# Performance work log

Hardware: AMD Instinct MI355X
Metric: run time of the kernel (lower is better)

The kernel has to match this reference:

```python
import jax, jax.numpy as jnp
import numpy as np

D = 1024
H = 16
DH = D // H  # 64
SCALE = DH ** (-0.5)

def setup_inputs() -> dict:
    key = jax.random.key(0)
    k1, k2, k3, k4, k5 = jax.random.split(key, 5)
    x = jax.random.normal(k1, (4, 2048, D), dtype=jnp.float32)
    w_qkv = jax.random.normal(k2, (D, 3 * D), dtype=jnp.float32) * (D ** -0.5)
    b_qkv = jax.random.normal(k3, (3 * D,), dtype=jnp.float32) * 0.02
    w_out = jax.random.normal(k4, (D, D), dtype=jnp.float32) * (D ** -0.5)
    b_out = jax.random.normal(k5, (D,), dtype=jnp.float32) * 0.02
    return {"x": x, "w_qkv": w_qkv, "b_qkv": b_qkv, "w_out": w_out, "b_out": b_out}

def reference(x, w_qkv, b_qkv, w_out, b_out):
    B, S, C = x.shape
    qkv = x @ w_qkv + b_qkv                          # [B,S,3D]
    qkv = qkv.reshape(B, S, 3, H, DH)
    qkv = jnp.transpose(qkv, (0, 3, 2, 1, 4))        # [B,H,3,S,DH]
    q, k, v = qkv[:, :, 0], qkv[:, :, 1], qkv[:, :, 2]
    q = q * SCALE
    scores = jnp.einsum('bhqd,bhkd->bhqk', q, k)     # [B,H,S,S]
    attn = jax.nn.softmax(scores.astype(jnp.float32), axis=-1).astype(scores.dtype)
    out = jnp.einsum('bhqk,bhkd->bhqd', attn, v)     # [B,H,S,DH]
    out = jnp.transpose(out, (0, 2, 1, 3)).reshape(B, S, C)
    return out @ w_out + b_out
```

## Files before the change

kernel.cpp:

```cpp
#include <hip/hip_runtime.h>

#define D_ 1024
#define H_ 16
#define DH_ 64
#define S_ 2048
#define B_ 4
#define N_ (B_*S_)
#define M3_ 3072
#define QSC_ 0.18033688011112042f

typedef _Float16 f16;
typedef _Float16 f16x8 __attribute__((ext_vector_type(8)));
typedef _Float16 f16x4 __attribute__((ext_vector_type(4)));
typedef _Float16 f16x2 __attribute__((ext_vector_type(2)));
typedef __fp16   h16x2 __attribute__((ext_vector_type(2)));
typedef float    f32x4 __attribute__((ext_vector_type(4)));

typedef __attribute__((address_space(1))) void gvoid;
typedef __attribute__((address_space(3))) void lvoid;

__device__ __forceinline__ void gl16(const f16* g, f16* l) {
    __builtin_amdgcn_global_load_lds((gvoid*)g, (lvoid*)l, 16, 0, 0);
}

__device__ __forceinline__ f16x2 pk_cvt(float a, float b) {
#if __has_builtin(__builtin_amdgcn_cvt_pkrtz)
    h16x2 t = __builtin_amdgcn_cvt_pkrtz(a, b);
    return __builtin_bit_cast(f16x2, t);
#else
    f16x2 r; r[0] = (f16)a; r[1] = (f16)b; return r;
#endif
}

__global__ __launch_bounds__(256) void cvt_x_kernel(const float* __restrict__ in,
                                                    f16* __restrict__ out) {
    size_t i = ((size_t)blockIdx.x * 256 + threadIdx.x) * 4;
    float4 f = *reinterpret_cast<const float4*>(in + i);
    f16x4 o;
    o[0] = (f16)f.x; o[1] = (f16)f.y; o[2] = (f16)f.z; o[3] = (f16)f.w;
    *reinterpret_cast<f16x4*>(out + i) = o;
}

__global__ __launch_bounds__(256) void wt_cvt_kernel(const float* __restrict__ in,
                                                     f16* __restrict__ out,
                                                     int K, int Nc) {
    __shared__ float tile[32][33];
    int tx = threadIdx.x & 31, ty = threadIdx.x >> 5;
    int c = blockIdx.x * 32 + tx;
    #pragma unroll
    for (int i = 0; i < 4; i++) {
        int r = blockIdx.y * 32 + ty + i * 8;
        tile[ty + i * 8][tx] = in[(size_t)r * Nc + c];
    }
    __syncthreads();
    #pragma unroll
    for (int i = 0; i < 4; i++) {
        int r2 = blockIdx.x * 32 + ty + i * 8;
        int c2 = blockIdx.y * 32 + tx;
        out[(size_t)r2 * K + c2] = (f16)tile[tx][ty + i * 8];
    }
}

__global__ __launch_bounds__(256) void gemm_qkv_kernel(
        const f16* __restrict__ A, const f16* __restrict__ Bt,
        const float* __restrict__ bias,
        f16* __restrict__ qo, f16* __restrict__ ko, f16* __restrict__ vTo) {
    __shared__ __align__(16) f16 As[128 * 32];
    __shared__ __align__(16) f16 Bs[128 * 32];
    const int tid  = threadIdx.x;
    const int lane = tid & 63, w = tid >> 6;
    const int quad = lane >> 4, lrow = lane & 15;
    const int wm = (w & 1) * 64, wn = (w >> 1) * 64;
    const int n0 = blockIdx.x * 128, m0 = blockIdx.y * 128;

    f32x4 acc[4][4];
    #pragma unroll
    for (int i = 0; i < 4; i++)
        #pragma unroll
        for (int j = 0; j < 4; j++) acc[i][j] = {0.f, 0.f, 0.f, 0.f};

    const int ar0 = tid >> 2, ap0 = tid & 3;
    const f16* Ag0 = A  + (size_t)(n0 + ar0) * D_ + ap0 * 8;
    const f16* Ag1 = Ag0 + (size_t)64 * D_;
    const f16* Bg0 = Bt + (size_t)(m0 + ar0) * D_ + ap0 * 8;
    const f16* Bg1 = Bg0 + (size_t)64 * D_;
    f16* Asl = As + tid * 8;
    f16* Bsl = Bs + tid * 8;

    for (int kt = 0; kt < D_ / 32; kt++) {
        gl16(Ag0 + kt * 32, Asl);
        gl16(Ag1 + kt * 32, Asl + 64 * 32);
        gl16(Bg0 + kt * 32, Bsl);
        gl16(Bg1 + kt * 32, Bsl + 64 * 32);
        __syncthreads();
        f16x8 af[4], bf[4];
        #pragma unroll
        for (int i = 0; i < 4; i++)
            af[i] = *reinterpret_cast<const f16x8*>(&As[(wm + i * 16 + lrow) * 32 + quad * 8]);
        #pragma unroll
        for (int j = 0; j < 4; j++)
            bf[j] = *reinterpret_cast<const f16x8*>(&Bs[(wn + j * 16 + lrow) * 32 + quad * 8]);
        #pragma unroll
        for (int i = 0; i < 4; i++)
            #pragma unroll
            for (int j = 0; j < 4; j++)
                acc[i][j] = __builtin_amdgcn_mfma_f32_16x16x32_f16(af[i], bf[j], acc[i][j], 0, 0, 0);
        __syncthreads();
    }

    #pragma unroll
    for (int j = 0; j < 4; j++) {
        int m   = m0 + wn + j * 16 + lrow;
        int sec = m >> 10;
        int hd  = m & 1023;
        int hh  = hd >> 6, d = hd & 63;
        float bb = bias[m];
        if (sec == 2) {
            #pragma unroll
            for (int i = 0; i < 4; i++) {
                int n = n0 + wm + i * 16 + quad * 4;
                int bidx = n >> 11, s = n & 2047;
                f16x4 o;
                #pragma unroll
                for (int r = 0; r < 4; r++) o[r] = (f16)(acc[i][j][r] + bb);
                *reinterpret_cast<f16x4*>(
                    &vTo[(((size_t)(bidx * H_ + hh)) * DH_ + d) * S_ + s]) = o;
            }
        } else {
            f16* dst = (sec == 0) ? qo : ko;
            float sc = (sec == 0) ? QSC_ : 1.0f;
            #pragma unroll
            for (int i = 0; i < 4; i++) {
                #pragma unroll
                for (int r = 0; r < 4; r++) {
                    int n = n0 + wm + i * 16 + quad * 4 + r;
                    int bidx = n >> 11, s = n & 2047;
                    dst[(((size_t)(bidx * H_ + hh)) * S_ + s) * DH_ + d] =
                        (f16)((acc[i][j][r] + bb) * sc);
                }
            }
        }
    }
}

__global__ __launch_bounds__(256, 4) void attn_kernel(
        const f16* __restrict__ q, const f16* __restrict__ k,
        const f16* __restrict__ vT, f16* __restrict__ ctx) {
    __shared__ __align__(16) f16 Ks[2][64 * 64];
    __shared__ __align__(16) f16 Vs[2][64 * 64];
    const int tid  = threadIdx.x;
    const int lane = tid & 63, w = tid >> 6;
    const int quad = lane >> 4, lrow = lane & 15;
    const int id = blockIdx.x;
    const int bh = id & 63;
    const int q0 = (id >> 6) * 128;
    const int b  = bh >> 4, h = bh & 15;
    const f16* qb = q  + (size_t)bh * S_ * DH_;
    const f16* kb = k  + (size_t)bh * S_ * DH_;
    const f16* vb = vT + (size_t)bh * DH_ * S_;

    f16x8 qf[2][2];
    #pragma unroll
    for (int f = 0; f < 2; f++)
        #pragma unroll
        for (int hf = 0; hf < 2; hf++)
            qf[f][hf] = *reinterpret_cast<const f16x8*>(
                qb + (size_t)(q0 + w * 32 + f * 16 + lrow) * DH_ + hf * 32 + quad * 8);

    f16x8 ones8;
    #pragma unroll
    for (int i = 0; i < 8; i++) ones8[i] = (f16)1.f;

    f32x4 lacc[2];
    f32x4 ot[2][4];
    #pragma unroll
    for (int f = 0; f < 2; f++) {
        lacc[f] = {0.f, 0.f, 0.f, 0.f};
        #pragma unroll
        for (int dj = 0; dj < 4; dj++) ot[f][dj] = {0.f, 0.f, 0.f, 0.f};
    }

    int koff[2], voff[2];
    #pragma unroll
    for (int i = 0; i < 2; i++) {
        int c = i * 256 + tid;
        int s = c >> 3, p = c & 7;
        int g = (s & ~31) | (((s >> 2) & 3) << 3) | (((s >> 4) & 1) << 2) | (s & 3);
        koff[i] = g * DH_ + ((p ^ (s & 7)) * 8);
        voff[i] = s * S_ + ((p ^ (s & 7)) * 8);
    }

    #pragma unroll
    for (int i = 0; i < 2; i++) {
        gl16(kb + koff[i], &Ks[0][(i * 256 + tid) * 8]);
        gl16(vb + voff[i], &Vs[0][(i * 256 + tid) * 8]);
    }
    __syncthreads();

    const int xr0 = (quad ^ (lrow & 7)) * 8;
    const int xr1 = ((quad + 4) ^ (lrow & 7)) * 8;

    union PU { f16x8 v; f16x2 w[4]; };

    const int NT = S_ / 64;
    for (int kt = 0; kt < NT; kt++) {
        const int cur = kt & 1;
        const f16* Kc = Ks[cur];
        const f16* Vc = Vs[cur];

        f32x4 st0[2][2];
        __builtin_amdgcn_s_setprio(1);
        #pragma unroll
        for (int half = 0; half < 2; half++) {
            const int rb = (half * 16 + lrow) * 64;
            const f16x8 k0 = *reinterpret_cast<const f16x8*>(&Kc[rb + xr0]);
            const f16x8 k1 = *reinterpret_cast<const f16x8*>(&Kc[rb + xr1]);
            #pragma unroll
            for (int f = 0; f < 2; f++) {
                f32x4 s = {0.f, 0.f, 0.f, 0.f};
                s = __builtin_amdgcn_mfma_f32_16x16x32_f16(k0, qf[f][0], s, 0, 0, 0);
                s = __builtin_amdgcn_mfma_f32_16x16x32_f16(k1, qf[f][1], s, 0, 0, 0);
                st0[half][f] = s;
            }
        }
        __builtin_amdgcn_s_setprio(0);

        if (kt + 1 < NT) {
            const size_t kv1 = (size_t)(kt + 1) * 64;
            #pragma unroll
            for (int i = 0; i < 2; i++) {
                gl16(kb + kv1 * DH_ + koff[i], &Ks[cur ^ 1][(i * 256 + tid) * 8]);
                gl16(vb + kv1 + voff[i],       &Vs[cur ^ 1][(i * 256 + tid) * 8]);
            }
        }

        PU p0[2];
        #pragma unroll
        for (int half = 0; half < 2; half++)
            #pragma unroll
            for (int f = 0; f < 2; f++) {
                f16x2 lo = pk_cvt(__builtin_amdgcn_exp2f(st0[half][f][0]),
                                  __builtin_amdgcn_exp2f(st0[half][f][1]));
                f16x2 hi = pk_cvt(__builtin_amdgcn_exp2f(st0[half][f][2]),
                                  __builtin_amdgcn_exp2f(st0[half][f][3]));
                p0[f].w[half * 2 + 0] = lo;
                p0[f].w[half * 2 + 1] = hi;
            }

        f32x4 st1[2][2];
        __builtin_amdgcn_s_setprio(1);
        #pragma unroll
        for (int half = 0; half < 2; half++) {
            const int rb = ((2 + half) * 16 + lrow) * 64;
            const f16x8 k0 = *reinterpret_cast<const f16x8*>(&Kc[rb + xr0]);
            const f16x8 k1 = *reinterpret_cast<const f16x8*>(&Kc[rb + xr1]);
            #pragma unroll
            for (int f = 0; f < 2; f++) {
                f32x4 s = {0.f, 0.f, 0.f, 0.f};
                s = __builtin_amdgcn_mfma_f32_16x16x32_f16(k0, qf[f][0], s, 0, 0, 0);
                s = __builtin_amdgcn_mfma_f32_16x16x32_f16(k1, qf[f][1], s, 0, 0, 0);
                st1[half][f] = s;
            }
        }
        __builtin_amdgcn_s_setprio(0);

        f16x8 vf0[4];
        #pragma unroll
        for (int dj = 0; dj < 4; dj++)
            vf0[dj] = *reinterpret_cast<const f16x8*>(
                &Vc[(dj * 16 + lrow) * 64 + ((quad ^ (lrow & 7)) * 8)]);

        __builtin_amdgcn_s_setprio(1);
        #pragma unroll
        for (int dj = 0; dj < 4; dj++)
            #pragma unroll
            for (int f = 0; f < 2; f++)
                ot[f][dj] = __builtin_amdgcn_mfma_f32_16x16x32_f16(vf0[dj], p0[f].v, ot[f][dj], 0, 0, 0);
        #pragma unroll
        for (int f = 0; f < 2; f++)
            lacc[f] = __builtin_amdgcn_mfma_f32_16x16x32_f16(ones8, p0[f].v, lacc[f], 0, 0, 0);
        __builtin_amdgcn_s_setprio(0);

        PU p1[2];
        #pragma unroll
        for (int half = 0; half < 2; half++)
            #pragma unroll
            for (int f = 0; f < 2; f++) {
                f16x2 lo = pk_cvt(__builtin_amdgcn_exp2f(st1[half][f][0]),
                                  __builtin_amdgcn_exp2f(st1[half][f][1]));
                f16x2 hi = pk_cvt(__builtin_amdgcn_exp2f(st1[half][f][2]),
                                  __builtin_amdgcn_exp2f(st1[half][f][3]));
                p1[f].w[half * 2 + 0] = lo;
                p1[f].w[half * 2 + 1] = hi;
            }

        f16x8 vf1[4];
        #pragma unroll
        for (int dj = 0; dj < 4; dj++)
            vf1[dj] = *reinterpret_cast<const f16x8*>(
                &Vc[(dj * 16 + lrow) * 64 + (((4 + quad) ^ (lrow & 7)) * 8)]);

        __builtin_amdgcn_s_setprio(1);
        #pragma unroll
        for (int dj = 0; dj < 4; dj++)
            #pragma unroll
            for (int f = 0; f < 2; f++)
                ot[f][dj] = __builtin_amdgcn_mfma_f32_16x16x32_f16(vf1[dj], p1[f].v, ot[f][dj], 0, 0, 0);
        #pragma unroll
        for (int f = 0; f < 2; f++)
            lacc[f] = __builtin_amdgcn_mfma_f32_16x16x32_f16(ones8, p1[f].v, lacc[f], 0, 0, 0);
        __builtin_amdgcn_s_setprio(0);

        __syncthreads();
    }

    #pragma unroll
    for (int f = 0; f < 2; f++) {
        float inv = 1.0f / lacc[f][0];
        int qrow = q0 + w * 32 + f * 16 + lrow;
        #pragma unroll
        for (int dj = 0; dj < 4; dj++) {
            f16x4 o;
            #pragma unroll
            for (int r = 0; r < 4; r++) o[r] = (f16)(ot[f][dj][r] * inv);
            *reinterpret_cast<f16x4*>(
                &ctx[((size_t)(b * S_ + qrow)) * D_ + h * DH_ + dj * 16 + quad * 4]) = o;
        }
    }
}

__global__ __launch_bounds__(256) void gemm_out_kernel(
        const f16* __restrict__ A, const f16* __restrict__ Bt,
        const float* __restrict__ bias, float* __restrict__ out) {
    __shared__ __align__(16) f16 As[128 * 32];
    __shared__ __align__(16) f16 Bs[128 * 32];
    const int tid  = threadIdx.x;
    const int lane = tid & 63, w = tid >> 6;
    const int quad = lane >> 4, lrow = lane & 15;
    const int wm = (w & 1) * 64, wn = (w >> 1) * 64;
    const int n0 = blockIdx.x * 128, m0 = blockIdx.y * 128;

    f32x4 acc[4][4];
    #pragma unroll
    for (int i = 0; i < 4; i++)
        #pragma unroll
        for (int j = 0; j < 4; j++) acc[i][j] = {0.f, 0.f, 0.f, 0.f};

    const int ar0 = tid >> 2, ap0 = tid & 3;
    const f16* Ag0 = A  + (size_t)(n0 + ar0) * D_ + ap0 * 8;
    const f16* Ag1 = Ag0 + (size_t)64 * D_;
    const f16* Bg0 = Bt + (size_t)(m0 + ar0) * D_ + ap0 * 8;
    const f16* Bg1 = Bg0 + (size_t)64 * D_;
    f16* Asl = As + tid * 8;
    f16* Bsl = Bs + tid * 8;

    for (int kt = 0; kt < D_ / 32; kt++) {
        gl16(Ag0 + kt * 32, Asl);
        gl16(Ag1 + kt * 32, Asl + 64 * 32);
        gl16(Bg0 + kt * 32, Bsl);
        gl16(Bg1 + kt * 32, Bsl + 64 * 32);
        __syncthreads();
        f16x8 af[4], bf[4];
        #pragma unroll
        for (int i = 0; i < 4; i++)
            af[i] = *reinterpret_cast<const f16x8*>(&As[(wm + i * 16 + lrow) * 32 + quad * 8]);
        #pragma unroll
        for (int j = 0; j < 4; j++)
            bf[j] = *reinterpret_cast<const f16x8*>(&Bs[(wn + j * 16 + lrow) * 32 + quad * 8]);
        #pragma unroll
        for (int i = 0; i < 4; i++)
            #pragma unroll
            for (int j = 0; j < 4; j++)
                acc[i][j] = __builtin_amdgcn_mfma_f32_16x16x32_f16(af[i], bf[j], acc[i][j], 0, 0, 0);
        __syncthreads();
    }

    #pragma unroll
    for (int j = 0; j < 4; j++) {
        int m = m0 + wn + j * 16 + lrow;
        float bb = bias[m];
        #pragma unroll
        for (int i = 0; i < 4; i++)
            #pragma unroll
            for (int r = 0; r < 4; r++) {
                int n = n0 + wm + i * 16 + quad * 4 + r;
                out[(size_t)n * D_ + m] = acc[i][j][r] + bb;
            }
    }
}

extern "C" void kernel_launch(void* const* d_in, const int* in_sizes, int n_in,
                              void* d_out, int out_size, void* d_ws, size_t ws_size,
                              hipStream_t stream) {
    (void)in_sizes; (void)n_in; (void)out_size; (void)ws_size;
    const float* x     = (const float*)d_in[0];
    const float* w_qkv = (const float*)d_in[1];
    const float* b_qkv = (const float*)d_in[2];
    const float* w_out = (const float*)d_in[3];
    const float* b_out = (const float*)d_in[4];
    float* out = (float*)d_out;

    char* ws = (char*)d_ws;
    const size_t MB = 1024 * 1024;
    f16* xb    = (f16*)(ws);
    f16* wqkvT = (f16*)(ws + 16 * MB);
    f16* woutT = (f16*)(ws + 22 * MB);
    f16* qs    = (f16*)(ws + 24 * MB);
    f16* kk    = (f16*)(ws + 40 * MB);
    f16* vTb   = (f16*)(ws + 72 * MB);
    f16* ctx   = xb;

    cvt_x_kernel<<<(N_ * D_) / (256 * 4), 256, 0, stream>>>(x, xb);
    wt_cvt_kernel<<<dim3(M3_ / 32, D_ / 32), 256, 0, stream>>>(w_qkv, wqkvT, D_, M3_);
    wt_cvt_kernel<<<dim3(D_ / 32, D_ / 32), 256, 0, stream>>>(w_out, woutT, D_, D_);
    gemm_qkv_kernel<<<dim3(N_ / 128, M3_ / 128), 256, 0, stream>>>(xb, wqkvT, b_qkv, qs, kk, vTb);
    attn_kernel<<<(B_ * H_) * (S_ / 128), 256, 0, stream>>>(qs, kk, vTb, ctx);
    gemm_out_kernel<<<dim3(N_ / 128, D_ / 128), 256, 0, stream>>>(ctx, woutT, b_out, out);
}
```

Baseline: 267.2 us.

## Rework QKV GEMM into 256x256 double-buffered pipeline with swizzled LDS

Reworks the QKV projection GEMM to use 256x256 output tiles with 512 threads. K tiles are double-buffered in LDS, and the global_load_lds prefetch of the next tile overlaps the MFMA work on the current one. LDS chunks are XOR-swizzled to avoid bank conflicts, the 1D block index is remapped for L2 locality, and s_setprio raises priority around the MFMA bursts. This removes the per-iteration full barrier stall and raises arithmetic intensity, in exchange for 128 KB of LDS and a 128-float accumulator per thread, which limits occupancy.

```diff
diff --git a/kernel.cpp b/kernel.cpp
--- a/kernel.cpp
+++ b/kernel.cpp
@@ -61,52 +61,109 @@
     }
 }
 
-__global__ __launch_bounds__(256) void gemm_qkv_kernel(
+__global__ __launch_bounds__(512, 2) void gemm_qkv_kernel(
         const f16* __restrict__ A, const f16* __restrict__ Bt,
         const float* __restrict__ bias,
         f16* __restrict__ qo, f16* __restrict__ ko, f16* __restrict__ vTo) {
-    __shared__ __align__(16) f16 As[128 * 32];
-    __shared__ __align__(16) f16 Bs[128 * 32];
+    __shared__ __align__(16) f16 S[2 * 4 * 8192];
     const int tid  = threadIdx.x;
     const int lane = tid & 63, w = tid >> 6;
     const int quad = lane >> 4, lrow = lane & 15;
-    const int wm = (w & 1) * 64, wn = (w >> 1) * 64;
-    const int n0 = blockIdx.x * 128, m0 = blockIdx.y * 128;
-
-    f32x4 acc[4][4];
-    #pragma unroll
-    for (int i = 0; i < 4; i++)
+    const int G  = w >> 2;
+    const int wn = (w & 3) * 64;
+
+    const int id  = blockIdx.x;
+    const int swz = (id & 7) * 48 + (id >> 3);
+    const int n0 = (swz & 31) * 256;
+    const int m0 = (swz >> 5) * 256;
+
+    f32x4 acc[8][4];
+    #pragma unroll
+    for (int i = 0; i < 8; i++)
         #pragma unroll
         for (int j = 0; j < 4; j++) acc[i][j] = {0.f, 0.f, 0.f, 0.f};
 
-    const int ar0 = tid >> 2, ap0 = tid & 3;
-    const f16* Ag0 = A  + (size_t)(n0 + ar0) * D_ + ap0 * 8;
-    const f16* Ag1 = Ag0 + (size_t)64 * D_;
-    const f16* Bg0 = Bt + (size_t)(m0 + ar0) * D_ + ap0 * 8;
-    const f16* Bg1 = Bg0 + (size_t)64 * D_;
-    f16* Asl = As + tid * 8;
-    f16* Bsl = Bs + tid * 8;
-
-    for (int kt = 0; kt < D_ / 32; kt++) {
-        gl16(Ag0 + kt * 32, Asl);
-        gl16(Ag1 + kt * 32, Asl + 64 * 32);
-        gl16(Bg0 + kt * 32, Bsl);
-        gl16(Bg1 + kt * 32, Bsl + 64 * 32);
-        __syncthreads();
-        f16x8 af[4], bf[4];
-        #pragma unroll
-        for (int i = 0; i < 4; i++)
-            af[i] = *reinterpret_cast<const f16x8*>(&As[(wm + i * 16 + lrow) * 32 + quad * 8]);
-        #pragma unroll
-        for (int j = 0; j < 4; j++)
-            bf[j] = *reinterpret_cast<const f16x8*>(&Bs[(wn + j * 16 + lrow) * 32 + quad * 8]);
-        #pragma unroll
-        for (int i = 0; i < 4; i++)
+    const int c0 = tid, c1 = tid + 512;
+    const int r0 = c0 >> 2, r1 = c1 >> 2;
+    const int g0 = r0 * D_ + (((c0 & 3) ^ (r0 & 3)) * 8);
+    const int g1 = r1 * D_ + (((c1 & 3) ^ (r1 & 3)) * 8);
+    const f16* Ab = A  + (size_t)n0 * D_;
+    const f16* Bb = Bt + (size_t)m0 * D_;
+
+    const int xq8   = (quad ^ (lrow & 3)) * 8;
+    const int abase = (G * 128 + lrow) * 32 + xq8;
+    const int bbase = (wn + lrow) * 32 + xq8;
+
+#define STAGE_QKV(ktn, ck, nb) do {                                          \
+    const int ko_ = (ktn) * 64 + (ck) * 32;                                  \
+    gl16(Ab + ko_ + g0, &S[(((nb) * 4 + (ck)) * 8192) + c0 * 8]);            \
+    gl16(Ab + ko_ + g1, &S[(((nb) * 4 + (ck)) * 8192) + c1 * 8]);            \
+    gl16(Bb + ko_ + g0, &S[(((nb) * 4 + 2 + (ck)) * 8192) + c0 * 8]);        \
+    gl16(Bb + ko_ + g1, &S[(((nb) * 4 + 2 + (ck)) * 8192) + c1 * 8]);        \
+} while (0)
+
+    STAGE_QKV(0, 0, 0);
+    STAGE_QKV(0, 1, 0);
+    asm volatile("s_waitcnt vmcnt(4)" ::: "memory");
+    __builtin_amdgcn_s_barrier();
+    __builtin_amdgcn_sched_barrier(0);
+
+    #pragma unroll 1
+    for (int kt = 0; kt < 15; kt++) {
+        const int buf = kt & 1, nb = buf ^ 1;
+        #pragma unroll
+        for (int ck = 0; ck < 2; ck++) {
+            const f16* Sa = &S[(buf * 4 + ck) * 8192];
+            const f16* Sb = &S[(buf * 4 + 2 + ck) * 8192];
+            f16x8 af[8], bf[4];
+            #pragma unroll
+            for (int i = 0; i < 8; i++)
+                af[i] = *reinterpret_cast<const f16x8*>(Sa + abase + i * 512);
             #pragma unroll
             for (int j = 0; j < 4; j++)
-                acc[i][j] = __builtin_amdgcn_mfma_f32_16x16x32_f16(af[i], bf[j], acc[i][j], 0, 0, 0);
-        __syncthreads();
-    }
+                bf[j] = *reinterpret_cast<const f16x8*>(Sb + bbase + j * 512);
+            STAGE_QKV(kt + 1, ck, nb);
+            __builtin_amdgcn_sched_barrier(0);
+            __builtin_amdgcn_s_setprio(1);
+            #pragma unroll
+            for (int i = 0; i < 8; i++)
+                #pragma unroll
+                for (int j = 0; j < 4; j++)
+                    acc[i][j] = __builtin_amdgcn_mfma_f32_16x16x32_f16(af[i], bf[j], acc[i][j], 0, 0, 0);
+            __builtin_amdgcn_s_setprio(0);
+            asm volatile("s_waitcnt vmcnt(4)" ::: "memory");
+            __builtin_amdgcn_s_barrier();
+            __builtin_amdgcn_sched_barrier(0);
+        }
+    }
+    {
+        const int buf = 1;
+        #pragma unroll
+        for (int ck = 0; ck < 2; ck++) {
+            const f16* Sa = &S[(buf * 4 + ck) * 8192];
+            const f16* Sb = &S[(buf * 4 + 2 + ck) * 8192];
+            f16x8 af[8], bf[4];
+            #pragma unroll
+            for (int i = 0; i < 8; i++)
+                af[i] = *reinterpret_cast<const f16x8*>(Sa + abase + i * 512);
+            #pragma unroll
+            for (int j = 0; j < 4; j++)
+                bf[j] = *reinterpret_cast<const f16x8*>(Sb + bbase + j * 512);
+            __builtin_amdgcn_s_setprio(1);
+            #pragma unroll
+            for (int i = 0; i < 8; i++)
+                #pragma unroll
+                for (int j = 0; j < 4; j++)
+                    acc[i][j] = __builtin_amdgcn_mfma_f32_16x16x32_f16(af[i], bf[j], acc[i][j], 0, 0, 0);
+            __builtin_amdgcn_s_setprio(0);
+            if (ck == 0) {
+                asm volatile("s_waitcnt vmcnt(0)" ::: "memory");
+                __builtin_amdgcn_s_barrier();
+                __builtin_amdgcn_sched_barrier(0);
+            }
+        }
+    }
+#undef STAGE_QKV
 
     #pragma unroll
     for (int j = 0; j < 4; j++) {
@@ -117,8 +174,8 @@
         float bb = bias[m];
         if (sec == 2) {
             #pragma unroll
-            for (int i = 0; i < 4; i++) {
-                int n = n0 + wm + i * 16 + quad * 4;
+            for (int i = 0; i < 8; i++) {
+                int n = n0 + G * 128 + i * 16 + quad * 4;
                 int bidx = n >> 11, s = n & 2047;
                 f16x4 o;
                 #pragma unroll
@@ -130,10 +187,10 @@
             f16* dst = (sec == 0) ? qo : ko;
             float sc = (sec == 0) ? QSC_ : 1.0f;
             #pragma unroll
-            for (int i = 0; i < 4; i++) {
+            for (int i = 0; i < 8; i++) {
                 #pragma unroll
                 for (int r = 0; r < 4; r++) {
-                    int n = n0 + wm + i * 16 + quad * 4 + r;
+                    int n = n0 + G * 128 + i * 16 + quad * 4 + r;
                     int bidx = n >> 11, s = n & 2047;
                     dst[(((size_t)(bidx * H_ + hh)) * S_ + s) * DH_ + d] =
                         (f16)((acc[i][j][r] + bb) * sc);
@@ -413,7 +470,7 @@
     cvt_x_kernel<<<(N_ * D_) / (256 * 4), 256, 0, stream>>>(x, xb);
     wt_cvt_kernel<<<dim3(M3_ / 32, D_ / 32), 256, 0, stream>>>(w_qkv, wqkvT, D_, M3_);
     wt_cvt_kernel<<<dim3(D_ / 32, D_ / 32), 256, 0, stream>>>(w_out, woutT, D_, D_);
-    gemm_qkv_kernel<<<dim3(N_ / 128, M3_ / 128), 256, 0, stream>>>(xb, wqkvT, b_qkv, qs, kk, vTb);
+    gemm_qkv_kernel<<<dim3((N_ / 256) * (M3_ / 256)), 512, 0, stream>>>(xb, wqkvT, b_qkv, qs, kk, vTb);
     attn_kernel<<<(B_ * H_) * (S_ / 128), 256, 0, stream>>>(qs, kk, vTb, ctx);
     gemm_out_kernel<<<dim3(N_ / 128, D_ / 128), 256, 0, stream>>>(ctx, woutT, b_out, out);
 }
```

Result: no change. 272.2 us (+1.9%).

## Double-buffer GEMM LDS tiles, remap blocks per XCD, and merge prep kernels

Applied to the files above, without the earlier changes.

Both GEMM kernels now use double-buffered LDS tiles. The next K-slice is issued via global_load_lds before the current slice's MFMAs, so there is one barrier per iteration instead of two. Blocks are remapped on a 1D grid so that each XCD handles a contiguous group of row tiles, which should improve L2 reuse. The three conversion kernels are merged into a single prep launch, and MFMA sections get s_setprio plus a launch_bounds occupancy hint. The trade-off is doubled LDS per block and a possible race, since the async prefetch writes the other buffer while there is no explicit wait before the barrier.

```diff
diff --git a/kernel.cpp b/kernel.cpp
--- a/kernel.cpp
+++ b/kernel.cpp
@@ -32,46 +32,58 @@
 #endif
 }
 
-__global__ __launch_bounds__(256) void cvt_x_kernel(const float* __restrict__ in,
-                                                    f16* __restrict__ out) {
-    size_t i = ((size_t)blockIdx.x * 256 + threadIdx.x) * 4;
-    float4 f = *reinterpret_cast<const float4*>(in + i);
-    f16x4 o;
-    o[0] = (f16)f.x; o[1] = (f16)f.y; o[2] = (f16)f.z; o[3] = (f16)f.w;
-    *reinterpret_cast<f16x4*>(out + i) = o;
-}
-
-__global__ __launch_bounds__(256) void wt_cvt_kernel(const float* __restrict__ in,
-                                                     f16* __restrict__ out,
-                                                     int K, int Nc) {
+__global__ __launch_bounds__(256) void prep_kernel(
+        const float* __restrict__ x,  f16* __restrict__ xb,
+        const float* __restrict__ wq, f16* __restrict__ wqT,
+        const float* __restrict__ wo, f16* __restrict__ woT) {
     __shared__ float tile[32][33];
+    const int bid = blockIdx.x;
+    if (bid < 8192) {
+        size_t i = ((size_t)bid * 256 + threadIdx.x) * 4;
+        float4 f = *reinterpret_cast<const float4*>(x + i);
+        f16x4 o;
+        o[0] = (f16)f.x; o[1] = (f16)f.y; o[2] = (f16)f.z; o[3] = (f16)f.w;
+        *reinterpret_cast<f16x4*>(xb + i) = o;
+        return;
+    }
+    const float* in; f16* out; int Nc, bx, by;
+    if (bid < 11264) {
+        int t = bid - 8192;  in = wq; out = wqT; Nc = M3_;
+        bx = t % 96; by = t / 96;
+    } else {
+        int t = bid - 11264; in = wo; out = woT; Nc = D_;
+        bx = t & 31; by = t >> 5;
+    }
     int tx = threadIdx.x & 31, ty = threadIdx.x >> 5;
-    int c = blockIdx.x * 32 + tx;
+    int c = bx * 32 + tx;
     #pragma unroll
     for (int i = 0; i < 4; i++) {
-        int r = blockIdx.y * 32 + ty + i * 8;
+        int r = by * 32 + ty + i * 8;
         tile[ty + i * 8][tx] = in[(size_t)r * Nc + c];
     }
     __syncthreads();
     #pragma unroll
     for (int i = 0; i < 4; i++) {
-        int r2 = blockIdx.x * 32 + ty + i * 8;
-        int c2 = blockIdx.y * 32 + tx;
-        out[(size_t)r2 * K + c2] = (f16)tile[tx][ty + i * 8];
-    }
-}
-
-__global__ __launch_bounds__(256) void gemm_qkv_kernel(
+        int r2 = bx * 32 + ty + i * 8;
+        int c2 = by * 32 + tx;
+        out[(size_t)r2 * D_ + c2] = (f16)tile[tx][ty + i * 8];
+    }
+}
+
+__global__ __launch_bounds__(256, 3) void gemm_qkv_kernel(
         const f16* __restrict__ A, const f16* __restrict__ Bt,
         const float* __restrict__ bias,
         f16* __restrict__ qo, f16* __restrict__ ko, f16* __restrict__ vTo) {
-    __shared__ __align__(16) f16 As[128 * 32];
-    __shared__ __align__(16) f16 Bs[128 * 32];
+    __shared__ __align__(16) f16 As[2][128 * 32];
+    __shared__ __align__(16) f16 Bs[2][128 * 32];
     const int tid  = threadIdx.x;
     const int lane = tid & 63, w = tid >> 6;
     const int quad = lane >> 4, lrow = lane & 15;
     const int wm = (w & 1) * 64, wn = (w >> 1) * 64;
-    const int n0 = blockIdx.x * 128, m0 = blockIdx.y * 128;
+    const int id  = blockIdx.x;
+    const int xcd = id & 7, idx = id >> 3;
+    const int n0 = (xcd * 8 + (idx & 7)) * 128;
+    const int m0 = (idx >> 3) * 128;
 
     f32x4 acc[4][4];
     #pragma unroll
@@ -84,27 +96,36 @@
     const f16* Ag1 = Ag0 + (size_t)64 * D_;
     const f16* Bg0 = Bt + (size_t)(m0 + ar0) * D_ + ap0 * 8;
     const f16* Bg1 = Bg0 + (size_t)64 * D_;
-    f16* Asl = As + tid * 8;
-    f16* Bsl = Bs + tid * 8;
-
-    for (int kt = 0; kt < D_ / 32; kt++) {
-        gl16(Ag0 + kt * 32, Asl);
-        gl16(Ag1 + kt * 32, Asl + 64 * 32);
-        gl16(Bg0 + kt * 32, Bsl);
-        gl16(Bg1 + kt * 32, Bsl + 64 * 32);
-        __syncthreads();
+
+    gl16(Ag0, &As[0][tid * 8]);
+    gl16(Ag1, &As[0][tid * 8 + 64 * 32]);
+    gl16(Bg0, &Bs[0][tid * 8]);
+    gl16(Bg1, &Bs[0][tid * 8 + 64 * 32]);
+    __syncthreads();
+
+    for (int kt = 0; kt < 32; kt++) {
+        const int cur = kt & 1;
+        if (kt + 1 < 32) {
+            const int ko = (kt + 1) * 32;
+            gl16(Ag0 + ko, &As[cur ^ 1][tid * 8]);
+            gl16(Ag1 + ko, &As[cur ^ 1][tid * 8 + 64 * 32]);
+            gl16(Bg0 + ko, &Bs[cur ^ 1][tid * 8]);
+            gl16(Bg1 + ko, &Bs[cur ^ 1][tid * 8 + 64 * 32]);
+        }
         f16x8 af[4], bf[4];
         #pragma unroll
         for (int i = 0; i < 4; i++)
-            af[i] = *reinterpret_cast<const f16x8*>(&As[(wm + i * 16 + lrow) * 32 + quad * 8]);
+            af[i] = *reinterpret_cast<const f16x8*>(&As[cur][(wm + i * 16 + lrow) * 32 + quad * 8]);
         #pragma unroll
         for (int j = 0; j < 4; j++)
-            bf[j] = *reinterpret_cast<const f16x8*>(&Bs[(wn + j * 16 + lrow) * 32 + quad * 8]);
+            bf[j] = *reinterpret_cast<const f16x8*>(&Bs[cur][(wn + j * 16 + lrow) * 32 + quad * 8]);
+        __builtin_amdgcn_s_setprio(1);
         #pragma unroll
         for (int i = 0; i < 4; i++)
             #pragma unroll
             for (int j = 0; j < 4; j++)
                 acc[i][j] = __builtin_amdgcn_mfma_f32_16x16x32_f16(af[i], bf[j], acc[i][j], 0, 0, 0);
+        __builtin_amdgcn_s_setprio(0);
         __syncthreads();
     }
 
@@ -329,16 +350,19 @@
     }
 }
 
-__global__ __launch_bounds__(256) void gemm_out_kernel(
+__global__ __launch_bounds__(256, 3) void gemm_out_kernel(
         const f16* __restrict__ A, const f16* __restrict__ Bt,
         const float* __restrict__ bias, float* __restrict__ out) {
-    __shared__ __align__(16) f16 As[128 * 32];
-    __shared__ __align__(16) f16 Bs[128 * 32];
+    __shared__ __align__(16) f16 As[2][128 * 32];
+    __shared__ __align__(16) f16 Bs[2][128 * 32];
     const int tid  = threadIdx.x;
     const int lane = tid & 63, w = tid >> 6;
     const int quad = lane >> 4, lrow = lane & 15;
     const int wm = (w & 1) * 64, wn = (w >> 1) * 64;
-    const int n0 = blockIdx.x * 128, m0 = blockIdx.y * 128;
+    const int id  = blockIdx.x;
+    const int xcd = id & 7, idx = id >> 3;
+    const int n0 = (xcd * 8 + (idx & 7)) * 128;
+    const int m0 = (idx >> 3) * 128;
 
     f32x4 acc[4][4];
     #pragma unroll
@@ -351,27 +375,36 @@
     const f16* Ag1 = Ag0 + (size_t)64 * D_;
     const f16* Bg0 = Bt + (size_t)(m0 + ar0) * D_ + ap0 * 8;
     const f16* Bg1 = Bg0 + (size_t)64 * D_;
-    f16* Asl = As + tid * 8;
-    f16* Bsl = Bs + tid * 8;
-
-    for (int kt = 0; kt < D_ / 32; kt++) {
-        gl16(Ag0 + kt * 32, Asl);
-        gl16(Ag1 + kt * 32, Asl + 64 * 32);
-        gl16(Bg0 + kt * 32, Bsl);
-        gl16(Bg1 + kt * 32, Bsl + 64 * 32);
-        __syncthreads();
+
+    gl16(Ag0, &As[0][tid * 8]);
+    gl16(Ag1, &As[0][tid * 8 + 64 * 32]);
+    gl16(Bg0, &Bs[0][tid * 8]);
+    gl16(Bg1, &Bs[0][tid * 8 + 64 * 32]);
+    __syncthreads();
+
+    for (int kt = 0; kt < 32; kt++) {
+        const int cur = kt & 1;
+        if (kt + 1 < 32) {
+            const int ko = (kt + 1) * 32;
+            gl16(Ag0 + ko, &As[cur ^ 1][tid * 8]);
+            gl16(Ag1 + ko, &As[cur ^ 1][tid * 8 + 64 * 32]);
+            gl16(Bg0 + ko, &Bs[cur ^ 1][tid * 8]);
+            gl16(Bg1 + ko, &Bs[cur ^ 1][tid * 8 + 64 * 32]);
+        }
         f16x8 af[4], bf[4];
         #pragma unroll
         for (int i = 0; i < 4; i++)
-            af[i] = *reinterpret_cast<const f16x8*>(&As[(wm + i * 16 + lrow) * 32 + quad * 8]);
+            af[i] = *reinterpret_cast<const f16x8*>(&As[cur][(wm + i * 16 + lrow) * 32 + quad * 8]);
         #pragma unroll
         for (int j = 0; j < 4; j++)
-            bf[j] = *reinterpret_cast<const f16x8*>(&Bs[(wn + j * 16 + lrow) * 32 + quad * 8]);
+            bf[j] = *reinterpret_cast<const f16x8*>(&Bs[cur][(wn + j * 16 + lrow) * 32 + quad * 8]);
+        __builtin_amdgcn_s_setprio(1);
         #pragma unroll
         for (int i = 0; i < 4; i++)
             #pragma unroll
             for (int j = 0; j < 4; j++)
                 acc[i][j] = __builtin_amdgcn_mfma_f32_16x16x32_f16(af[i], bf[j], acc[i][j], 0, 0, 0);
+        __builtin_amdgcn_s_setprio(0);
         __syncthreads();
     }
 
@@ -410,10 +443,8 @@
     f16* vTb   = (f16*)(ws + 72 * MB);
     f16* ctx   = xb;
 
-    cvt_x_kernel<<<(N_ * D_) / (256 * 4), 256, 0, stream>>>(x, xb);
-    wt_cvt_kernel<<<dim3(M3_ / 32, D_ / 32), 256, 0, stream>>>(w_qkv, wqkvT, D_, M3_);
-    wt_cvt_kernel<<<dim3(D_ / 32, D_ / 32), 256, 0, stream>>>(w_out, woutT, D_, D_);
-    gemm_qkv_kernel<<<dim3(N_ / 128, M3_ / 128), 256, 0, stream>>>(xb, wqkvT, b_qkv, qs, kk, vTb);
+    prep_kernel<<<12288, 256, 0, stream>>>(x, xb, w_qkv, wqkvT, w_out, woutT);
+    gemm_qkv_kernel<<<1536, 256, 0, stream>>>(xb, wqkvT, b_qkv, qs, kk, vTb);
     attn_kernel<<<(B_ * H_) * (S_ / 128), 256, 0, stream>>>(qs, kk, vTb, ctx);
-    gemm_out_kernel<<<dim3(N_ / 128, D_ / 128), 256, 0, stream>>>(ctx, woutT, b_out, out);
-}
+    gemm_out_kernel<<<512, 256, 0, stream>>>(ctx, woutT, b_out, out);
+}
```

After: 268.8 us. About the same (+0.6%).
